# Kernel optimization log

Measured on AMD Instinct MI355X. Metric: run time of the kernel, lower is better.

The kernel has to match this reference:

```python
import jax, jax.numpy as jnp
import numpy as np

B, S, D, H = 8, 1024, 1024, 8
d = D // H  # d_spl = 128


def setup_inputs() -> dict:
    key = jax.random.key(0)
    ks = jax.random.split(key, 12)
    s = 0.02
    return {
        "q": jax.random.normal(ks[0], (B, S, D), jnp.float32),
        "k": jax.random.normal(ks[1], (B, S, D), jnp.float32),
        "v": jax.random.normal(ks[2], (B, S, D), jnp.float32),
        "mask": jax.random.randint(ks[3], (B, S), 0, 2).astype(jnp.int32),
        "Wq": jax.random.normal(ks[4], (D, D), jnp.float32) * s,
        "bq": jnp.zeros((D,), jnp.float32),
        "Wk": jax.random.normal(ks[5], (D, D), jnp.float32) * s,
        "bk": jnp.zeros((D,), jnp.float32),
        "Wv": jax.random.normal(ks[6], (D, D), jnp.float32) * s,
        "bv": jnp.zeros((D,), jnp.float32),
        "Wo": jax.random.normal(ks[7], (d, d), jnp.float32) * s,  # shared per-head out proj
        "bo": jnp.zeros((d,), jnp.float32),
    }


def reference(q, k, v, mask, Wq, bq, Wk, bk, Wv, bv, Wo, bo):
    Bq, Sq, Dm = q.shape
    dh = Dm // H
    # input projections (torch Linear: x @ W.T + b)
    qp = (q @ Wq.T + bq).reshape(Bq, Sq, H, dh)
    kp = (k @ Wk.T + bk).reshape(Bq, Sq, H, dh)
    vp = (v @ Wv.T + bv).reshape(Bq, Sq, H, dh)
    # per-head scaled scores: [B,H,S,S]
    scores = jnp.einsum('bqhd,bkhd->bhqk', qp, kp) / jnp.sqrt(jnp.asarray(dh, qp.dtype))
    # masked_fill(mask==0, -1e9); mask broadcasts over query dim (keys masked)
    scores = jnp.where(mask[:, None, None, :] == 0, jnp.asarray(-1e9, scores.dtype), scores)
    attn = jax.nn.softmax(scores, axis=-1)
    ctx = jnp.einsum('bhqk,bkhd->bqhd', attn, vp)  # [B,S,H,d]
    # shared per-head output linear (d_spl -> d_spl)
    out = jnp.einsum('bqhd,ed->bqhe', ctx, Wo) + bo
    output = out.reshape(Bq, Sq, Dm)
    # module returns PRE-softmax masked scores concatenated head-wise on dim 2:
    # cat([ [B,S,S] ] * H, dim=2) == transpose to [B,q,H,k] then reshape [B,S,H*S]
    raw_weights = jnp.transpose(scores, (0, 2, 1, 3)).reshape(Bq, Sq, H * Sq)
    return (output, raw_weights)
```

## Files before the change

### kernel.cpp

```cpp
#include <hip/hip_runtime.h>
#include <math.h>

#define B_ 8
#define S_ 1024
#define D_ 1024
#define H_ 8

typedef __bf16 bf16;
typedef __attribute__((ext_vector_type(8))) __bf16 bf16x8;
typedef __attribute__((ext_vector_type(4))) float f32x4;

#define MFMA16(a, b, c) __builtin_amdgcn_mfma_f32_16x16x32_bf16((a), (b), (c), 0, 0, 0)
#define GLOAD_LDS16(src, dst)                                                            \
    __builtin_amdgcn_global_load_lds((const __attribute__((address_space(1))) void*)(src), \
                                     (__attribute__((address_space(3))) void*)(dst), 16, 0, 0)

__global__ __launch_bounds__(256) void cast6(
    const float* __restrict__ q, const float* __restrict__ k, const float* __restrict__ v,
    const float* __restrict__ Wq, const float* __restrict__ Wk, const float* __restrict__ Wv,
    bf16* __restrict__ xq, bf16* __restrict__ xk, bf16* __restrict__ xv,
    bf16* __restrict__ wq, bf16* __restrict__ wk, bf16* __restrict__ wv)
{
    int t = blockIdx.y;
    const float* src;
    bf16* dst;
    size_t n;
    switch (t) {
        case 0: src = q;  dst = xq; n = 8388608; break;
        case 1: src = k;  dst = xk; n = 8388608; break;
        case 2: src = v;  dst = xv; n = 8388608; break;
        case 3: src = Wq; dst = wq; n = 1048576; break;
        case 4: src = Wk; dst = wk; n = 1048576; break;
        default: src = Wv; dst = wv; n = 1048576; break;
    }
    size_t i0 = ((size_t)blockIdx.x * 256 + threadIdx.x) * 8;
    if (i0 >= n) return;
    f32x4 a = *(const f32x4*)(src + i0);
    f32x4 b = *(const f32x4*)(src + i0 + 4);
    bf16x8 o;
#pragma unroll
    for (int j = 0; j < 4; ++j) { o[j] = (bf16)a[j]; o[4 + j] = (bf16)b[j]; }
    *(bf16x8*)(dst + i0) = o;
}

__global__ __launch_bounds__(256) void proj_bf16(
    const bf16* __restrict__ X, const bf16* __restrict__ W,
    const float* __restrict__ bias, bf16* __restrict__ out)
{
    __shared__ __align__(16) bf16 ldsA[128 * 64];
    __shared__ __align__(16) bf16 ldsB[128 * 64];
    const int tid  = threadIdx.x;
    const int lane = tid & 63;
    const int l15  = lane & 15, l4 = lane >> 4;
    const int wave = tid >> 6;
    const int wr   = wave >> 1, wc = wave & 1;

    int f   = blockIdx.x;
    int xcd = f & 7, idx = f >> 3;
    const int m0 = (xcd * 8 + (idx >> 3)) * 128;
    const int n0 = (idx & 7) * 128;

    f32x4 acc[4][4];
#pragma unroll
    for (int i = 0; i < 4; ++i)
#pragma unroll
        for (int j = 0; j < 4; ++j) acc[i][j] = (f32x4){0.f, 0.f, 0.f, 0.f};

    const int srow = lane >> 3, sch = lane & 7;

    for (int k0 = 0; k0 < 1024; k0 += 64) {
#pragma unroll
        for (int i = 0; i < 4; ++i) {
            int seg = wave * 4 + i;
            int row = seg * 8 + srow;
            GLOAD_LDS16(X + (size_t)(m0 + row) * 1024 + k0 + sch * 8, &ldsA[seg * 512]);
            GLOAD_LDS16(W + (size_t)(n0 + row) * 1024 + k0 + sch * 8, &ldsB[seg * 512]);
        }
        __syncthreads();
#pragma unroll
        for (int ks = 0; ks < 2; ++ks) {
            bf16x8 af[4], bfr[4];
            int ch = ks * 4 + l4;
#pragma unroll
            for (int mi = 0; mi < 4; ++mi)
                af[mi] = *(const bf16x8*)&ldsA[(wr * 64 + mi * 16 + l15) * 64 + ch * 8];
#pragma unroll
            for (int ni = 0; ni < 4; ++ni)
                bfr[ni] = *(const bf16x8*)&ldsB[(wc * 64 + ni * 16 + l15) * 64 + ch * 8];
#pragma unroll
            for (int mi = 0; mi < 4; ++mi)
#pragma unroll
                for (int ni = 0; ni < 4; ++ni)
                    acc[mi][ni] = MFMA16(af[mi], bfr[ni], acc[mi][ni]);
        }
        __syncthreads();
    }
#pragma unroll
    for (int ni = 0; ni < 4; ++ni) {
        int n = n0 + wc * 64 + ni * 16 + l15;
        float bval = bias[n];
#pragma unroll
        for (int mi = 0; mi < 4; ++mi)
#pragma unroll
            for (int r = 0; r < 4; ++r) {
                int m = m0 + wr * 64 + mi * 16 + l4 * 4 + r;
                out[(size_t)m * 1024 + n] = (bf16)(acc[mi][ni][r] + bval);
            }
    }
}

__global__ __launch_bounds__(256) void transpose_v(
    const bf16* __restrict__ vp, bf16* __restrict__ vpT)
{
    __shared__ __align__(16) bf16 t[64][80];
    const int tid = threadIdx.x;
    const int s0 = blockIdx.x * 64;
    const int db = blockIdx.y * 64;
    const int bh = blockIdx.z;
    const int b = bh >> 3, h = bh & 7;
#pragma unroll
    for (int rep = 0; rep < 2; ++rep) {
        int r = rep * 32 + (tid >> 3);
        int c = (tid & 7) * 8;
        *(bf16x8*)&t[r][c] =
            *(const bf16x8*)(vp + (size_t)(b * 1024 + s0 + r) * 1024 + h * 128 + db + c);
    }
    __syncthreads();
#pragma unroll
    for (int rep = 0; rep < 2; ++rep) {
        int dd = rep * 32 + (tid >> 3);
        int sc = (tid & 7) * 8;
        bf16x8 o;
#pragma unroll
        for (int j = 0; j < 8; ++j) o[j] = t[sc + j][dd];
        *(bf16x8*)(vpT + (size_t)((b * 8 + h) * 128 + db + dd) * 1024 + s0 + sc) = o;
    }
}

__global__ __launch_bounds__(256) void attn_kernel(
    const bf16* __restrict__ qp, const bf16* __restrict__ kp,
    const bf16* __restrict__ vpT, const int* __restrict__ mask,
    const float* __restrict__ Wo, const float* __restrict__ bo,
    float* __restrict__ out0, float* __restrict__ raw)
{
    __shared__ __align__(16) bf16 ldsK[64 * 128];
    __shared__ __align__(16) bf16 ldsV[128 * 64];
    __shared__ __align__(16) bf16 ldsP[4][16 * 64];

    const int tid  = threadIdx.x;
    const int lane = tid & 63;
    const int l15  = lane & 15, l4 = lane >> 4;
    const int wave = tid >> 6;

    int f = blockIdx.x;
    int xcd = f & 7, idx = f >> 3;
    int pair = xcd + 8 * (idx >> 4);
    int qt = idx & 15;
    int h = pair & 7, b = pair >> 3;
    const int q0 = qt * 64 + wave * 16;

    bf16x8 qf[4];
    const bf16* qbase = qp + (size_t)(b * 1024 + q0 + l15) * 1024 + h * 128 + l4 * 8;
#pragma unroll
    for (int ks = 0; ks < 4; ++ks) qf[ks] = *(const bf16x8*)(qbase + ks * 32);

    f32x4 ctx[8];
#pragma unroll
    for (int i = 0; i < 8; ++i) ctx[i] = (f32x4){0.f, 0.f, 0.f, 0.f};
    float m_run[4] = {-INFINITY, -INFINITY, -INFINITY, -INFINITY};
    float l_run[4] = {0.f, 0.f, 0.f, 0.f};

    const bf16* kbase_g = kp + (size_t)(b * 1024) * 1024 + h * 128;
    const bf16* vbase_g = vpT + (size_t)(b * 8 + h) * 128 * 1024;

    bf16x8 kreg[4], vreg[4];
    int mreg[4];
    auto load_tile = [&](int KB) {
#pragma unroll
        for (int j = 0; j < 4; ++j) {
            int fl = j * 256 + tid, rw = fl >> 4, ch = fl & 15;
            kreg[j] = *(const bf16x8*)(kbase_g + (size_t)(KB + rw) * 1024 + ch * 8);
        }
#pragma unroll
        for (int j = 0; j < 4; ++j) {
            int fl = j * 256 + tid, rw = fl >> 3, ch = fl & 7;
            vreg[j] = *(const bf16x8*)(vbase_g + (size_t)rw * 1024 + KB + ch * 8);
        }
#pragma unroll
        for (int nf = 0; nf < 4; ++nf) mreg[nf] = mask[b * 1024 + KB + nf * 16 + l15];
    };
    load_tile(0);

    const float scale = 0.08838834764831845f;

    for (int t = 0; t < 16; ++t) {
        const int kb = t * 64;
        __syncthreads();
#pragma unroll
        for (int j = 0; j < 4; ++j) {
            int fl = j * 256 + tid, rw = fl >> 4, ch = fl & 15;
            *(bf16x8*)&ldsK[rw * 128 + ((ch ^ (rw & 7)) << 3)] = kreg[j];
        }
#pragma unroll
        for (int j = 0; j < 4; ++j) {
            int fl = j * 256 + tid, rw = fl >> 3, ch = fl & 7;
            *(bf16x8*)&ldsV[rw * 64 + ((ch ^ (rw & 7)) << 3)] = vreg[j];
        }
        int msave[4];
#pragma unroll
        for (int nf = 0; nf < 4; ++nf) msave[nf] = mreg[nf];
        __syncthreads();
        if (t < 15) load_tile(kb + 64);

        f32x4 s[4];
        __builtin_amdgcn_s_setprio(1);
#pragma unroll
        for (int nf = 0; nf < 4; ++nf) {
            int row = nf * 16 + l15;
            f32x4 a = (f32x4){0.f, 0.f, 0.f, 0.f};
#pragma unroll
            for (int ks = 0; ks < 4; ++ks) {
                bf16x8 kf = *(const bf16x8*)&ldsK[row * 128 + (((ks * 4 + l4) ^ (row & 7)) << 3)];
                a = MFMA16(qf[ks], kf, a);
            }
#pragma unroll
            for (int r = 0; r < 4; ++r) s[nf][r] = msave[nf] ? a[r] * scale : -1e9f;
        }
        __builtin_amdgcn_s_setprio(0);
#pragma unroll
        for (int nf = 0; nf < 4; ++nf) {
            int key = kb + nf * 16 + l15;
#pragma unroll
            for (int r = 0; r < 4; ++r)
                raw[(size_t)(b * 1024 + q0 + l4 * 4 + r) * 8192 + h * 1024 + key] = s[nf][r];
        }
#pragma unroll
        for (int r = 0; r < 4; ++r) {
            float pm = fmaxf(fmaxf(s[0][r], s[1][r]), fmaxf(s[2][r], s[3][r]));
            pm = fmaxf(pm, __shfl_xor(pm, 1));
            pm = fmaxf(pm, __shfl_xor(pm, 2));
            pm = fmaxf(pm, __shfl_xor(pm, 4));
            pm = fmaxf(pm, __shfl_xor(pm, 8));
            float mn = fmaxf(m_run[r], pm);
            float alpha = __expf(m_run[r] - mn);
            m_run[r] = mn;
            float rs = 0.f;
#pragma unroll
            for (int nf = 0; nf < 4; ++nf) {
                float p = __expf(s[nf][r] - mn);
                s[nf][r] = p;
                rs += p;
            }
            rs += __shfl_xor(rs, 1);
            rs += __shfl_xor(rs, 2);
            rs += __shfl_xor(rs, 4);
            rs += __shfl_xor(rs, 8);
            l_run[r] = l_run[r] * alpha + rs;
#pragma unroll
            for (int df = 0; df < 8; ++df) ctx[df][r] *= alpha;
        }
#pragma unroll
        for (int nf = 0; nf < 4; ++nf)
#pragma unroll
            for (int r = 0; r < 4; ++r) {
                int qw = l4 * 4 + r;
                int keyl = nf * 16 + l15;
                int chw = keyl >> 3;
                ldsP[wave][qw * 64 + ((chw ^ (qw & 7)) << 3) + (keyl & 7)] = (bf16)s[nf][r];
            }
        __builtin_amdgcn_s_setprio(1);
#pragma unroll
        for (int kstep = 0; kstep < 2; ++kstep) {
            bf16x8 pf = *(const bf16x8*)&ldsP[wave][l15 * 64 + (((kstep * 4 + l4) ^ (l15 & 7)) << 3)];
#pragma unroll
            for (int df = 0; df < 8; ++df) {
                int row = df * 16 + l15;
                bf16x8 vf = *(const bf16x8*)&ldsV[row * 64 + (((kstep * 4 + l4) ^ (row & 7)) << 3)];
                ctx[df] = MFMA16(pf, vf, ctx[df]);
            }
        }
        __builtin_amdgcn_s_setprio(0);
    }

    __syncthreads();
    bf16* cbuf = &ldsK[wave * 2048];
    float invl[4];
#pragma unroll
    for (int r = 0; r < 4; ++r) invl[r] = 1.0f / l_run[r];
#pragma unroll
    for (int df = 0; df < 8; ++df)
#pragma unroll
        for (int r = 0; r < 4; ++r) {
            int qw = l4 * 4 + r;
            int dcol = df * 16 + l15;
            int chw = dcol >> 3;
            cbuf[qw * 128 + ((chw ^ (qw & 7)) << 3) + (dcol & 7)] = (bf16)(ctx[df][r] * invl[r]);
        }
    f32x4 oacc[8];
#pragma unroll
    for (int i = 0; i < 8; ++i) oacc[i] = (f32x4){0.f, 0.f, 0.f, 0.f};
#pragma unroll
    for (int ks = 0; ks < 4; ++ks) {
        int ch = ks * 4 + l4;
        bf16x8 cf = *(const bf16x8*)&cbuf[l15 * 128 + ((ch ^ (l15 & 7)) << 3)];
#pragma unroll
        for (int ef = 0; ef < 8; ++ef) {
            const float* wsrc = Wo + (ef * 16 + l15) * 128 + ks * 32 + l4 * 8;
            bf16x8 wf;
#pragma unroll
            for (int j = 0; j < 8; ++j) wf[j] = (bf16)wsrc[j];
            oacc[ef] = MFMA16(cf, wf, oacc[ef]);
        }
    }
#pragma unroll
    for (int ef = 0; ef < 8; ++ef) {
        float bias = bo[ef * 16 + l15];
#pragma unroll
        for (int r = 0; r < 4; ++r) {
            int qrow = q0 + l4 * 4 + r;
            out0[(size_t)(b * 1024 + qrow) * 1024 + h * 128 + ef * 16 + l15] =
                oacc[ef][r] + bias;
        }
    }
}

extern "C" void kernel_launch(void* const* d_in, const int* in_sizes, int n_in,
                              void* d_out, int out_size, void* d_ws, size_t ws_size,
                              hipStream_t stream) {
    const float* q    = (const float*)d_in[0];
    const float* k    = (const float*)d_in[1];
    const float* v    = (const float*)d_in[2];
    const int*   mask = (const int*)d_in[3];
    const float* Wq   = (const float*)d_in[4];
    const float* bq   = (const float*)d_in[5];
    const float* Wk   = (const float*)d_in[6];
    const float* bk   = (const float*)d_in[7];
    const float* Wv   = (const float*)d_in[8];
    const float* bv   = (const float*)d_in[9];
    const float* Wo   = (const float*)d_in[10];
    const float* bo   = (const float*)d_in[11];

    float* out0 = (float*)d_out;
    float* raw  = out0 + (size_t)B_ * S_ * D_;

    char* rb = (char*)raw;
    bf16* xq  = (bf16*)(rb);
    bf16* xk  = (bf16*)(rb + (size_t)16 * 1048576);
    bf16* xv  = (bf16*)(rb + (size_t)32 * 1048576);
    bf16* wqb = (bf16*)(rb + (size_t)48 * 1048576);
    bf16* wkb = (bf16*)(rb + (size_t)50 * 1048576);
    bf16* wvb = (bf16*)(rb + (size_t)52 * 1048576);
    bf16* vp  = (bf16*)(rb + (size_t)54 * 1048576);

    bf16* qp  = (bf16*)d_ws;
    bf16* kp  = qp + (size_t)8388608;
    bf16* vpT = kp + (size_t)8388608;

    cast6<<<dim3(4096, 6), 256, 0, stream>>>(q, k, v, Wq, Wk, Wv, xq, xk, xv, wqb, wkb, wvb);
    proj_bf16<<<512, 256, 0, stream>>>(xq, wqb, bq, qp);
    proj_bf16<<<512, 256, 0, stream>>>(xk, wkb, bk, kp);
    proj_bf16<<<512, 256, 0, stream>>>(xv, wvb, bv, vp);
    transpose_v<<<dim3(16, 2, 64), 256, 0, stream>>>(vp, vpT);
    attn_kernel<<<1024, 256, 0, stream>>>(qp, kp, vpT, mask, Wo, bo, out0, raw);
}
```

Measured before the change: 638.4 us.

## Rewrite attention with 32x32 MFMA, register-resident P, lazy rescale; merge projections

Attention now runs on 32x32x16 MFMAs with 32 query rows per wave, computing S^T so each lane owns one query row. The P and ctx fragments are built with cross-half lane shuffles instead of LDS round-trips. Raw scores are written with vector stores, and the online-softmax rescale is skipped unless the max grows by more than 8. The three projection GEMMs are merged into one launch, with the softmax scale folded into the Q projection. These changes aim to cut LDS traffic, scattered raw-score stores and launch overhead. The costs are higher register pressure with occupancy capped at 2 blocks, and Q rounded to bf16 after scaling.

```diff
diff --git a/kernel.cpp b/kernel.cpp
--- a/kernel.cpp
+++ b/kernel.cpp
@@ -9,8 +9,10 @@
 typedef __bf16 bf16;
 typedef __attribute__((ext_vector_type(8))) __bf16 bf16x8;
 typedef __attribute__((ext_vector_type(4))) float f32x4;
+typedef __attribute__((ext_vector_type(16))) float f32x16;
 
 #define MFMA16(a, b, c) __builtin_amdgcn_mfma_f32_16x16x32_bf16((a), (b), (c), 0, 0, 0)
+#define MFMA32(a, b, c) __builtin_amdgcn_mfma_f32_32x32x16_bf16((a), (b), (c), 0, 0, 0)
 #define GLOAD_LDS16(src, dst)                                                            \
     __builtin_amdgcn_global_load_lds((const __attribute__((address_space(1))) void*)(src), \
                                      (__attribute__((address_space(3))) void*)(dst), 16, 0, 0)
@@ -43,9 +45,11 @@
     *(bf16x8*)(dst + i0) = o;
 }
 
-__global__ __launch_bounds__(256) void proj_bf16(
-    const bf16* __restrict__ X, const bf16* __restrict__ W,
-    const float* __restrict__ bias, bf16* __restrict__ out)
+__global__ __launch_bounds__(256) void proj3(
+    const bf16* Xq, const bf16* Xk, const bf16* Xv,
+    const bf16* Wqp, const bf16* Wkp, const bf16* Wvp,
+    const float* bq, const float* bk, const float* bv,
+    bf16* oq, bf16* ok, bf16* ov, float qscale)
 {
     __shared__ __align__(16) bf16 ldsA[128 * 64];
     __shared__ __align__(16) bf16 ldsB[128 * 64];
@@ -55,8 +59,15 @@
     const int wave = tid >> 6;
     const int wr   = wave >> 1, wc = wave & 1;
 
-    int f   = blockIdx.x;
-    int xcd = f & 7, idx = f >> 3;
+    int f = blockIdx.x;
+    int xcd = f & 7, r = f >> 3;
+    int which = r >> 6, idx = r & 63;
+    const bf16* X = which == 0 ? Xq : (which == 1 ? Xk : Xv);
+    const bf16* W = which == 0 ? Wqp : (which == 1 ? Wkp : Wvp);
+    const float* bias = which == 0 ? bq : (which == 1 ? bk : bv);
+    bf16* out = which == 0 ? oq : (which == 1 ? ok : ov);
+    const float scale = which == 0 ? qscale : 1.0f;
+
     const int m0 = (xcd * 8 + (idx >> 3)) * 128;
     const int n0 = (idx & 7) * 128;
 
@@ -102,9 +113,9 @@
 #pragma unroll
         for (int mi = 0; mi < 4; ++mi)
 #pragma unroll
-            for (int r = 0; r < 4; ++r) {
-                int m = m0 + wr * 64 + mi * 16 + l4 * 4 + r;
-                out[(size_t)m * 1024 + n] = (bf16)(acc[mi][ni][r] + bval);
+            for (int rr = 0; rr < 4; ++rr) {
+                int m = m0 + wr * 64 + mi * 16 + l4 * 4 + rr;
+                out[(size_t)m * 1024 + n] = (bf16)((acc[mi][ni][rr] + bval) * scale);
             }
     }
 }
@@ -137,191 +148,230 @@
     }
 }
 
-__global__ __launch_bounds__(256) void attn_kernel(
+__global__ __launch_bounds__(256, 2) void attn_kernel(
     const bf16* __restrict__ qp, const bf16* __restrict__ kp,
     const bf16* __restrict__ vpT, const int* __restrict__ mask,
     const float* __restrict__ Wo, const float* __restrict__ bo,
     float* __restrict__ out0, float* __restrict__ raw)
 {
     __shared__ __align__(16) bf16 ldsK[64 * 128];
-    __shared__ __align__(16) bf16 ldsV[128 * 64];
-    __shared__ __align__(16) bf16 ldsP[4][16 * 64];
+    __shared__ __align__(16) bf16 ldsV[64 * 128];
 
     const int tid  = threadIdx.x;
     const int lane = tid & 63;
-    const int l15  = lane & 15, l4 = lane >> 4;
+    const int l31  = lane & 31;
+    const int hi   = lane >> 5;
     const int wave = tid >> 6;
 
     int f = blockIdx.x;
     int xcd = f & 7, idx = f >> 3;
-    int pair = xcd + 8 * (idx >> 4);
-    int qt = idx & 15;
+    int pair = xcd + 8 * (idx >> 3);
+    int qt = idx & 7;
     int h = pair & 7, b = pair >> 3;
-    const int q0 = qt * 64 + wave * 16;
-
-    bf16x8 qf[4];
-    const bf16* qbase = qp + (size_t)(b * 1024 + q0 + l15) * 1024 + h * 128 + l4 * 8;
-#pragma unroll
-    for (int ks = 0; ks < 4; ++ks) qf[ks] = *(const bf16x8*)(qbase + ks * 32);
-
-    f32x4 ctx[8];
-#pragma unroll
-    for (int i = 0; i < 8; ++i) ctx[i] = (f32x4){0.f, 0.f, 0.f, 0.f};
-    float m_run[4] = {-INFINITY, -INFINITY, -INFINITY, -INFINITY};
-    float l_run[4] = {0.f, 0.f, 0.f, 0.f};
-
-    const bf16* kbase_g = kp + (size_t)(b * 1024) * 1024 + h * 128;
-    const bf16* vbase_g = vpT + (size_t)(b * 8 + h) * 128 * 1024;
+    const int ql = qt * 128 + wave * 32 + l31;
+
+    bf16x8 qf[8];
+    const bf16* qrow = qp + (size_t)(b * 1024 + ql) * 1024 + h * 128 + hi * 8;
+#pragma unroll
+    for (int ds = 0; ds < 8; ++ds) qf[ds] = *(const bf16x8*)(qrow + ds * 16);
+
+    f32x16 ctx[4];
+#pragma unroll
+    for (int dt = 0; dt < 4; ++dt)
+#pragma unroll
+        for (int i = 0; i < 16; ++i) ctx[dt][i] = 0.f;
+    float m_run = -INFINITY, l_run = 0.f;
+
+    const bf16* kbase = kp + (size_t)(b * 1024) * 1024 + h * 128;
+    const bf16* vbase = vpT + (size_t)((b * 8 + h) * 128) * 1024;
 
     bf16x8 kreg[4], vreg[4];
-    int mreg[4];
-    auto load_tile = [&](int KB) {
+    auto prefetch = [&](int KB) {
 #pragma unroll
         for (int j = 0; j < 4; ++j) {
-            int fl = j * 256 + tid, rw = fl >> 4, ch = fl & 15;
-            kreg[j] = *(const bf16x8*)(kbase_g + (size_t)(KB + rw) * 1024 + ch * 8);
+            int fl = j * 256 + tid;
+            kreg[j] = *(const bf16x8*)(kbase + (size_t)(KB + (fl >> 4)) * 1024 + (fl & 15) * 8);
         }
 #pragma unroll
         for (int j = 0; j < 4; ++j) {
-            int fl = j * 256 + tid, rw = fl >> 3, ch = fl & 7;
-            vreg[j] = *(const bf16x8*)(vbase_g + (size_t)rw * 1024 + KB + ch * 8);
-        }
-#pragma unroll
-        for (int nf = 0; nf < 4; ++nf) mreg[nf] = mask[b * 1024 + KB + nf * 16 + l15];
+            int fl = j * 256 + tid;
+            vreg[j] = *(const bf16x8*)(vbase + (size_t)(fl >> 3) * 1024 + KB + (fl & 7) * 8);
+        }
     };
-    load_tile(0);
-
-    const float scale = 0.08838834764831845f;
+    prefetch(0);
 
     for (int t = 0; t < 16; ++t) {
         const int kb = t * 64;
         __syncthreads();
 #pragma unroll
         for (int j = 0; j < 4; ++j) {
-            int fl = j * 256 + tid, rw = fl >> 4, ch = fl & 15;
-            *(bf16x8*)&ldsK[rw * 128 + ((ch ^ (rw & 7)) << 3)] = kreg[j];
+            int fl = j * 256 + tid;
+            int row = fl >> 4, c = fl & 15;
+            *(bf16x8*)&ldsK[row * 128 + ((c ^ (row & 15)) << 3)] = kreg[j];
         }
 #pragma unroll
         for (int j = 0; j < 4; ++j) {
-            int fl = j * 256 + tid, rw = fl >> 3, ch = fl & 7;
-            *(bf16x8*)&ldsV[rw * 64 + ((ch ^ (rw & 7)) << 3)] = vreg[j];
-        }
-        int msave[4];
-#pragma unroll
-        for (int nf = 0; nf < 4; ++nf) msave[nf] = mreg[nf];
+            int fl = j * 256 + tid;
+            int d = fl >> 3, c8 = fl & 7;
+            int lr = d >> 1, c = ((d & 1) << 3) | c8;
+            *(bf16x8*)&ldsV[lr * 128 + ((c ^ (lr & 15)) << 3)] = vreg[j];
+        }
         __syncthreads();
-        if (t < 15) load_tile(kb + 64);
-
-        f32x4 s[4];
+        if (t < 15) prefetch(kb + 64);
+
+        f32x16 sa[2];
+#pragma unroll
+        for (int mt = 0; mt < 2; ++mt)
+#pragma unroll
+            for (int i = 0; i < 16; ++i) sa[mt][i] = 0.f;
         __builtin_amdgcn_s_setprio(1);
 #pragma unroll
-        for (int nf = 0; nf < 4; ++nf) {
-            int row = nf * 16 + l15;
-            f32x4 a = (f32x4){0.f, 0.f, 0.f, 0.f};
+        for (int mt = 0; mt < 2; ++mt) {
+            int row = mt * 32 + l31;
+#pragma unroll
+            for (int ds = 0; ds < 8; ++ds) {
+                int c = 2 * ds + hi;
+                bf16x8 kf = *(const bf16x8*)&ldsK[row * 128 + ((c ^ (row & 15)) << 3)];
+                sa[mt] = MFMA32(kf, qf[ds], sa[mt]);
+            }
+        }
+        __builtin_amdgcn_s_setprio(0);
+
+        float s[2][16];
+        float* rawrow = raw + (size_t)(b * 1024 + ql) * 8192 + h * 1024 + kb;
+#pragma unroll
+        for (int mt = 0; mt < 2; ++mt)
+#pragma unroll
+            for (int r1 = 0; r1 < 4; ++r1) {
+                int koff = mt * 32 + r1 * 8 + hi * 4;
+                int4 mv = *(const int4*)(mask + b * 1024 + kb + koff);
+                s[mt][r1 * 4 + 0] = mv.x ? sa[mt][r1 * 4 + 0] : -1e9f;
+                s[mt][r1 * 4 + 1] = mv.y ? sa[mt][r1 * 4 + 1] : -1e9f;
+                s[mt][r1 * 4 + 2] = mv.z ? sa[mt][r1 * 4 + 2] : -1e9f;
+                s[mt][r1 * 4 + 3] = mv.w ? sa[mt][r1 * 4 + 3] : -1e9f;
+                f32x4 st = {s[mt][r1 * 4 + 0], s[mt][r1 * 4 + 1],
+                            s[mt][r1 * 4 + 2], s[mt][r1 * 4 + 3]};
+                *(f32x4*)(rawrow + koff) = st;
+            }
+
+        float pm = s[0][0];
+#pragma unroll
+        for (int mt = 0; mt < 2; ++mt)
+#pragma unroll
+            for (int i = 0; i < 16; ++i) pm = fmaxf(pm, s[mt][i]);
+        pm = fmaxf(pm, __shfl_xor(pm, 32));
+        if (!__all(pm <= m_run + 8.0f)) {
+            float mn = fmaxf(m_run, pm);
+            float al = __expf(m_run - mn);
+#pragma unroll
+            for (int dt = 0; dt < 4; ++dt)
+#pragma unroll
+                for (int i = 0; i < 16; ++i) ctx[dt][i] *= al;
+            l_run *= al;
+            m_run = mn;
+        }
+        float ps = 0.f;
+#pragma unroll
+        for (int mt = 0; mt < 2; ++mt)
+#pragma unroll
+            for (int i = 0; i < 16; ++i) {
+                float p = __expf(s[mt][i] - m_run);
+                s[mt][i] = p;
+                ps += p;
+            }
+        ps += __shfl_xor(ps, 32);
+        l_run += ps;
+
+        bf16x8 pfrag[4];
+#pragma unroll
+        for (int mt = 0; mt < 2; ++mt)
+#pragma unroll
+            for (int sub = 0; sub < 2; ++sub) {
+                float sv[4], rv[4];
+#pragma unroll
+                for (int j = 0; j < 4; ++j)
+                    sv[j] = hi ? s[mt][sub * 8 + j] : s[mt][sub * 8 + 4 + j];
+#pragma unroll
+                for (int j = 0; j < 4; ++j) rv[j] = __shfl_xor(sv[j], 32);
+                bf16x8 pf;
+#pragma unroll
+                for (int j = 0; j < 4; ++j) {
+                    pf[j]     = (bf16)(hi ? rv[j] : s[mt][sub * 8 + j]);
+                    pf[4 + j] = (bf16)(hi ? s[mt][sub * 8 + 4 + j] : rv[j]);
+                }
+                pfrag[mt * 2 + sub] = pf;
+            }
+
+        __builtin_amdgcn_s_setprio(1);
+#pragma unroll
+        for (int dt = 0; dt < 4; ++dt) {
+            int d0 = dt * 32 + l31;
+            int lr = d0 >> 1, cb = (d0 & 1) << 3;
 #pragma unroll
             for (int ks = 0; ks < 4; ++ks) {
-                bf16x8 kf = *(const bf16x8*)&ldsK[row * 128 + (((ks * 4 + l4) ^ (row & 7)) << 3)];
-                a = MFMA16(qf[ks], kf, a);
-            }
-#pragma unroll
-            for (int r = 0; r < 4; ++r) s[nf][r] = msave[nf] ? a[r] * scale : -1e9f;
+                int c = cb | (ks * 2 + hi);
+                bf16x8 vf = *(const bf16x8*)&ldsV[lr * 128 + ((c ^ (lr & 15)) << 3)];
+                ctx[dt] = MFMA32(vf, pfrag[ks], ctx[dt]);
+            }
         }
         __builtin_amdgcn_s_setprio(0);
-#pragma unroll
-        for (int nf = 0; nf < 4; ++nf) {
-            int key = kb + nf * 16 + l15;
-#pragma unroll
-            for (int r = 0; r < 4; ++r)
-                raw[(size_t)(b * 1024 + q0 + l4 * 4 + r) * 8192 + h * 1024 + key] = s[nf][r];
-        }
-#pragma unroll
-        for (int r = 0; r < 4; ++r) {
-            float pm = fmaxf(fmaxf(s[0][r], s[1][r]), fmaxf(s[2][r], s[3][r]));
-            pm = fmaxf(pm, __shfl_xor(pm, 1));
-            pm = fmaxf(pm, __shfl_xor(pm, 2));
-            pm = fmaxf(pm, __shfl_xor(pm, 4));
-            pm = fmaxf(pm, __shfl_xor(pm, 8));
-            float mn = fmaxf(m_run[r], pm);
-            float alpha = __expf(m_run[r] - mn);
-            m_run[r] = mn;
-            float rs = 0.f;
-#pragma unroll
-            for (int nf = 0; nf < 4; ++nf) {
-                float p = __expf(s[nf][r] - mn);
-                s[nf][r] = p;
-                rs += p;
-            }
-            rs += __shfl_xor(rs, 1);
-            rs += __shfl_xor(rs, 2);
-            rs += __shfl_xor(rs, 4);
-            rs += __shfl_xor(rs, 8);
-            l_run[r] = l_run[r] * alpha + rs;
-#pragma unroll
-            for (int df = 0; df < 8; ++df) ctx[df][r] *= alpha;
-        }
-#pragma unroll
-        for (int nf = 0; nf < 4; ++nf)
-#pragma unroll
-            for (int r = 0; r < 4; ++r) {
-                int qw = l4 * 4 + r;
-                int keyl = nf * 16 + l15;
-                int chw = keyl >> 3;
-                ldsP[wave][qw * 64 + ((chw ^ (qw & 7)) << 3) + (keyl & 7)] = (bf16)s[nf][r];
-            }
-        __builtin_amdgcn_s_setprio(1);
-#pragma unroll
-        for (int kstep = 0; kstep < 2; ++kstep) {
-            bf16x8 pf = *(const bf16x8*)&ldsP[wave][l15 * 64 + (((kstep * 4 + l4) ^ (l15 & 7)) << 3)];
-#pragma unroll
-            for (int df = 0; df < 8; ++df) {
-                int row = df * 16 + l15;
-                bf16x8 vf = *(const bf16x8*)&ldsV[row * 64 + (((kstep * 4 + l4) ^ (row & 7)) << 3)];
-                ctx[df] = MFMA16(pf, vf, ctx[df]);
-            }
-        }
-        __builtin_amdgcn_s_setprio(0);
-    }
-
-    __syncthreads();
-    bf16* cbuf = &ldsK[wave * 2048];
-    float invl[4];
-#pragma unroll
-    for (int r = 0; r < 4; ++r) invl[r] = 1.0f / l_run[r];
-#pragma unroll
-    for (int df = 0; df < 8; ++df)
-#pragma unroll
-        for (int r = 0; r < 4; ++r) {
-            int qw = l4 * 4 + r;
-            int dcol = df * 16 + l15;
-            int chw = dcol >> 3;
-            cbuf[qw * 128 + ((chw ^ (qw & 7)) << 3) + (dcol & 7)] = (bf16)(ctx[df][r] * invl[r]);
-        }
-    f32x4 oacc[8];
-#pragma unroll
-    for (int i = 0; i < 8; ++i) oacc[i] = (f32x4){0.f, 0.f, 0.f, 0.f};
-#pragma unroll
-    for (int ks = 0; ks < 4; ++ks) {
-        int ch = ks * 4 + l4;
-        bf16x8 cf = *(const bf16x8*)&cbuf[l15 * 128 + ((ch ^ (l15 & 7)) << 3)];
-#pragma unroll
-        for (int ef = 0; ef < 8; ++ef) {
-            const float* wsrc = Wo + (ef * 16 + l15) * 128 + ks * 32 + l4 * 8;
+    }
+
+    float invl = 1.0f / l_run;
+#pragma unroll
+    for (int dt = 0; dt < 4; ++dt)
+#pragma unroll
+        for (int i = 0; i < 16; ++i) ctx[dt][i] *= invl;
+
+    bf16x8 cb[8];
+#pragma unroll
+    for (int dt = 0; dt < 4; ++dt)
+#pragma unroll
+        for (int sub = 0; sub < 2; ++sub) {
+            float sv[4], rv[4];
+#pragma unroll
+            for (int j = 0; j < 4; ++j)
+                sv[j] = hi ? ctx[dt][sub * 8 + j] : ctx[dt][sub * 8 + 4 + j];
+#pragma unroll
+            for (int j = 0; j < 4; ++j) rv[j] = __shfl_xor(sv[j], 32);
+            bf16x8 cf;
+#pragma unroll
+            for (int j = 0; j < 4; ++j) {
+                cf[j]     = (bf16)(hi ? rv[j] : ctx[dt][sub * 8 + j]);
+                cf[4 + j] = (bf16)(hi ? ctx[dt][sub * 8 + 4 + j] : rv[j]);
+            }
+            cb[dt * 2 + sub] = cf;
+        }
+
+    f32x16 oacc[4];
+#pragma unroll
+    for (int et = 0; et < 4; ++et)
+#pragma unroll
+        for (int i = 0; i < 16; ++i) oacc[et][i] = 0.f;
+#pragma unroll
+    for (int et = 0; et < 4; ++et) {
+        const float* wr = Wo + (et * 32 + l31) * 128 + hi * 8;
+#pragma unroll
+        for (int dsub = 0; dsub < 8; ++dsub) {
+            f32x4 w0 = *(const f32x4*)(wr + dsub * 16);
+            f32x4 w1 = *(const f32x4*)(wr + dsub * 16 + 4);
             bf16x8 wf;
 #pragma unroll
-            for (int j = 0; j < 8; ++j) wf[j] = (bf16)wsrc[j];
-            oacc[ef] = MFMA16(cf, wf, oacc[ef]);
-        }
-    }
-#pragma unroll
-    for (int ef = 0; ef < 8; ++ef) {
-        float bias = bo[ef * 16 + l15];
-#pragma unroll
-        for (int r = 0; r < 4; ++r) {
-            int qrow = q0 + l4 * 4 + r;
-            out0[(size_t)(b * 1024 + qrow) * 1024 + h * 128 + ef * 16 + l15] =
-                oacc[ef][r] + bias;
-        }
-    }
+            for (int j = 0; j < 4; ++j) { wf[j] = (bf16)w0[j]; wf[4 + j] = (bf16)w1[j]; }
+            oacc[et] = MFMA32(wf, cb[dsub], oacc[et]);
+        }
+    }
+    float* orow = out0 + (size_t)(b * 1024 + ql) * 1024 + h * 128;
+#pragma unroll
+    for (int et = 0; et < 4; ++et)
+#pragma unroll
+        for (int r1 = 0; r1 < 4; ++r1) {
+            int eb = et * 32 + r1 * 8 + hi * 4;
+            f32x4 bo4 = *(const f32x4*)(bo + eb);
+            f32x4 st = {oacc[et][r1 * 4 + 0] + bo4[0], oacc[et][r1 * 4 + 1] + bo4[1],
+                        oacc[et][r1 * 4 + 2] + bo4[2], oacc[et][r1 * 4 + 3] + bo4[3]};
+            *(f32x4*)(orow + eb) = st;
+        }
 }
 
 extern "C" void kernel_launch(void* const* d_in, const int* in_sizes, int n_in,
@@ -356,10 +406,11 @@
     bf16* kp  = qp + (size_t)8388608;
     bf16* vpT = kp + (size_t)8388608;
 
+    const float scale = 0.08838834764831845f;
+
     cast6<<<dim3(4096, 6), 256, 0, stream>>>(q, k, v, Wq, Wk, Wv, xq, xk, xv, wqb, wkb, wvb);
-    proj_bf16<<<512, 256, 0, stream>>>(xq, wqb, bq, qp);
-    proj_bf16<<<512, 256, 0, stream>>>(xk, wkb, bk, kp);
-    proj_bf16<<<512, 256, 0, stream>>>(xv, wvb, bv, vp);
+    proj3<<<1536, 256, 0, stream>>>(xq, xk, xv, wqb, wkb, wvb, bq, bk, bv,
+                                    qp, kp, vp, scale);
     transpose_v<<<dim3(16, 2, 64), 256, 0, stream>>>(vp, vpT);
-    attn_kernel<<<1024, 256, 0, stream>>>(qp, kp, vpT, mask, Wo, bo, out0, raw);
+    attn_kernel<<<512, 256, 0, stream>>>(qp, kp, vpT, mask, Wo, bo, out0, raw);
 }
```

Result: faster. 581.4 us (-8.9%).
